# Performance work log

Hardware: AMD Instinct MI355X
Metric: run time of the kernel (lower is better)

## Reference

```python
import jax, jax.numpy as jnp
import numpy as np

N, K = 8192, 32
DIM_INP_Q, DIM_INP_KV, DIM, DIM_OUT = 256, 256, 256, 512


def setup_inputs() -> dict:
    key = jax.random.key(0)
    ks = jax.random.split(key, 16)
    s = lambda k_, shp: jax.random.normal(k_, shp, dtype=jnp.float32) * 0.05
    return {
        "xyz_q": jax.random.normal(ks[0], (N, 3), dtype=jnp.float32),
        "feats_q": jax.random.normal(ks[1], (N, DIM_INP_Q), dtype=jnp.float32),
        "xyz_kv": jax.random.normal(ks[2], (N, K, 3), dtype=jnp.float32),
        "feats_kv": jax.random.normal(ks[3], (N, K, DIM_INP_KV), dtype=jnp.float32),
        # linear weights stored (in, out); y = x @ W + b
        "Wq": s(ks[4], (DIM_INP_Q, DIM)),
        "Wk": s(ks[5], (DIM_INP_KV, DIM)),
        "Wv": s(ks[6], (DIM_INP_KV, DIM)),
        "d1_w": s(ks[7], (3, DIM // 2)), "d1_b": jnp.zeros((DIM // 2,), jnp.float32),
        "d2_w": s(ks[8], (DIM // 2, DIM)), "d2_b": jnp.zeros((DIM,), jnp.float32),
        "g1_w": s(ks[9], (DIM, DIM)), "g1_b": jnp.zeros((DIM,), jnp.float32),
        "g2_w": s(ks[10], (DIM, DIM)), "g2_b": jnp.zeros((DIM,), jnp.float32),
        "out_w": s(ks[11], (DIM, DIM_OUT)), "out_b": jnp.zeros((DIM_OUT,), jnp.float32),
    }


def reference(xyz_q, feats_q, xyz_kv, feats_kv, Wq, Wk, Wv,
              d1_w, d1_b, d2_w, d2_b, g1_w, g1_b, g2_w, g2_b, out_w, out_b):
    q_attn = feats_q @ Wq                      # (N, dim)
    k_attn = feats_kv @ Wk                     # (N, k, dim)
    v_attn = feats_kv @ Wv                     # (N, k, dim)
    # relative-position MLP: (N, k, 3) -> (N, k, dim)
    rel = xyz_q[:, None, :] - xyz_kv
    pos_encode = jax.nn.relu(rel @ d1_w + d1_b) @ d2_w + d2_b
    # subtractive vector attention scores through fc_gamma MLP
    h = q_attn[:, None, :] - k_attn + pos_encode
    attn = jax.nn.relu(h @ g1_w + g1_b) @ g2_w + g2_b   # (N, k, dim)
    attn = jax.nn.softmax(attn, axis=-2)                # softmax over neighbors k
    res = jnp.einsum('nmf,nmf->nf', attn, v_attn + pos_encode)
    res = res @ out_w + out_b                           # (N, dim_out)
    return (xyz_q, res)
```

## Files before the change

### kernel.cpp

```cpp
#include <hip/hip_runtime.h>
#include <hip/hip_bf16.h>

#define NPTS 8192
#define KN   32
#define DIM  256
#define DH   128
#define DOUT 512

typedef __attribute__((ext_vector_type(8))) short bf16x8;
typedef __attribute__((ext_vector_type(4))) short short4v;
typedef __attribute__((ext_vector_type(4))) float f32x4;

#define MFMA16(a, b, c) __builtin_amdgcn_mfma_f32_16x16x32_bf16((a), (b), (c), 0, 0, 0)

__device__ __forceinline__ short f2b(float f) {
    __hip_bfloat16 h = __float2bfloat16(f);
    return *reinterpret_cast<short*>(&h);
}

#define WSO_QATTN 0u
#define WSO_RES   8388608u
#define WSO_WKT   16777216u
#define WSO_WVT   16908288u
#define WSO_G1T   17039360u
#define WSO_G2T   17170432u
#define WSO_D2T   17301504u
#define WSO_OWT   17367040u

extern "C" __global__ __launch_bounds__(256)
void prep_w(const float* __restrict__ Wk, const float* __restrict__ Wv,
            const float* __restrict__ g1w, const float* __restrict__ g2w,
            const float* __restrict__ d2w, const float* __restrict__ ow,
            short* __restrict__ wkT, short* __restrict__ wvT,
            short* __restrict__ g1T, short* __restrict__ g2T,
            short* __restrict__ d2T, short* __restrict__ owT)
{
    const int idx = blockIdx.x * 256 + threadIdx.x;
    if (idx < 65536) {
        const int o = idx >> 8, i = idx & 255;
        wkT[idx] = f2b(-Wk[i * 256 + o]);
        wvT[idx] = f2b(Wv[i * 256 + o]);
        g1T[idx] = f2b(g1w[i * 256 + o]);
        g2T[idx] = f2b(g2w[i * 256 + o]);
    }
    if (idx < 32768) {
        const int o = idx >> 7, i = idx & 127;
        d2T[idx] = f2b(d2w[i * 256 + o]);
    }
    if (idx < 131072) {
        const int o = idx >> 8, i = idx & 255;
        owT[idx] = f2b(ow[i * 512 + o]);
    }
}

extern "C" __global__ __launch_bounds__(256)
void prep_q(const float* __restrict__ feats_q, const float* __restrict__ Wq,
            const float* __restrict__ xyz_q, float* __restrict__ q_attn,
            float* __restrict__ out)
{
    const int b = blockIdx.x;
    const int t = threadIdx.x;
    if (b >= 512) {
        const int idx = (b - 512) * 256 + t;
        out[idx] = xyz_q[idx];
        return;
    }
    __shared__ float s_q[16][256];
    for (int j = 0; j < 16; ++j)
        s_q[j][t] = feats_q[(size_t)(b * 16 + j) * 256 + t];
    __syncthreads();
    float acc[16];
    #pragma unroll
    for (int pt = 0; pt < 16; ++pt) acc[pt] = 0.f;
    for (int k = 0; k < 256; ++k) {
        const float wv = Wq[k * 256 + t];
        #pragma unroll
        for (int pt = 0; pt < 16; ++pt) acc[pt] = fmaf(s_q[pt][k], wv, acc[pt]);
    }
    #pragma unroll
    for (int pt = 0; pt < 16; ++pt)
        q_attn[(size_t)(b * 16 + pt) * 256 + t] = acc[pt];
}


#define STAGE_FEATS(koff)                                                         \
    {                                                                             \
        const float* fp_ = feats_kv + ((size_t)p0 * KN + srow) * DIM + (koff) +   \
                           scs * 32;                                              \
        _Pragma("unroll")                                                         \
        for (int j_ = 0; j_ < 8; ++j_) {                                          \
            const float4 v_ = *(const float4*)(fp_ + 4 * j_);                     \
            const int c2_ = scs * 32 + 4 * j_;                                    \
            short4v t_;                                                           \
            t_[0] = f2b(v_.x); t_[1] = f2b(v_.y);                                 \
            t_[2] = f2b(v_.z); t_[3] = f2b(v_.w);                                 \
            *(short4v*)&s_lds[srow * 128 + (c2_ ^ ((srow & 7) << 3))] = t_;       \
        }                                                                         \
    }

extern "C" __global__ __launch_bounds__(512, 2)
void ctb_main(const float* __restrict__ xyz_q, const float* __restrict__ xyz_kv,
              const float* __restrict__ feats_kv,
              const float* __restrict__ d1w, const float* __restrict__ d1b,
              const float* __restrict__ d2b, const float* __restrict__ g1b,
              const float* __restrict__ g2b,
              const float* __restrict__ q_attn,
              const short* __restrict__ wkTn, const short* __restrict__ wvT,
              const short* __restrict__ g1T, const short* __restrict__ g2T,
              const short* __restrict__ d2T,
              float* __restrict__ res_ws)
{
    extern __shared__ short s_lds[];
    const int t    = threadIdx.x;
    const int w    = t >> 6;
    const int lane = t & 63;
    const int q    = lane >> 4;
    const int ln   = lane & 15;
    const int p0   = blockIdx.x * 4;
    const int colbase = 32 * w + ln;

    const int srow = t >> 2;
    const int scs  = t & 3;

    STAGE_FEATS(0);
    {
        const int pt = srow >> 5;
        const float qx = xyz_q[(p0 + pt) * 3 + 0];
        const float qy = xyz_q[(p0 + pt) * 3 + 1];
        const float qz = xyz_q[(p0 + pt) * 3 + 2];
        const float* xk = xyz_kv + ((size_t)p0 * KN + srow) * 3;
        const float rx = qx - xk[0], ry = qy - xk[1], rz = qz - xk[2];
        #pragma unroll
        for (int j = 0; j < 32; ++j) {
            const int c = scs * 32 + j;
            const float v = fmaxf(fmaf(rx, d1w[c],
                                  fmaf(ry, d1w[DH + c],
                                  fmaf(rz, d1w[2 * DH + c], d1b[c]))), 0.f);
            s_lds[16384 + srow * 128 + (c ^ ((srow & 7) << 3))] = f2b(v);
        }
    }
    __syncthreads();

    f32x4 vp[8][2];
    #pragma unroll
    for (int nt = 0; nt < 2; ++nt) {
        const float bb = d2b[colbase + 16 * nt];
        #pragma unroll
        for (int mt = 0; mt < 8; ++mt) vp[mt][nt] = (f32x4){bb, bb, bb, bb};
    }
    #pragma unroll
    for (int ks = 0; ks < 4; ++ks) {
        bf16x8 ar[8];
        #pragma unroll
        for (int mt = 0; mt < 8; ++mt) {
            const int row = 16 * mt + ln;
            ar[mt] = *(const bf16x8*)&s_lds[16384 + row * 128 +
                                            ((32 * ks + 8 * q) ^ ((row & 7) << 3))];
        }
        #pragma unroll
        for (int nt = 0; nt < 2; ++nt) {
            const bf16x8 bb = *(const bf16x8*)(d2T + (colbase + 16 * nt) * DH +
                                               32 * ks + 8 * q);
            #pragma unroll
            for (int mt = 0; mt < 8; ++mt)
                vp[mt][nt] = MFMA16(ar[mt], bb, vp[mt][nt]);
        }
    }
    f32x4 hacc[8][2];
    #pragma unroll
    for (int nt = 0; nt < 2; ++nt)
        #pragma unroll
        for (int pt = 0; pt < 4; ++pt) {
            const float qv = q_attn[(size_t)(p0 + pt) * DIM + colbase + 16 * nt];
            #pragma unroll
            for (int m2 = 0; m2 < 2; ++m2) {
                const int mt = 2 * pt + m2;
                #pragma unroll
                for (int r = 0; r < 4; ++r) hacc[mt][nt][r] = vp[mt][nt][r] + qv;
            }
        }
    #pragma unroll
    for (int half = 0; half < 2; ++half) {
        if (half) {
            __syncthreads();
            STAGE_FEATS(128);
            __syncthreads();
        }
        #pragma unroll
        for (int ksl = 0; ksl < 4; ++ksl) {
            const int ks = 4 * half + ksl;
            bf16x8 af[8];
            #pragma unroll
            for (int mt = 0; mt < 8; ++mt) {
                const int row = 16 * mt + ln;
                af[mt] = *(const bf16x8*)&s_lds[row * 128 +
                                                ((32 * ksl + 8 * q) ^ ((row & 7) << 3))];
            }
            #pragma unroll
            for (int nt = 0; nt < 2; ++nt) {
                const int co = (colbase + 16 * nt) * DIM + 32 * ks + 8 * q;
                const bf16x8 bk = *(const bf16x8*)(wkTn + co);
                const bf16x8 bv = *(const bf16x8*)(wvT + co);
                #pragma unroll
                for (int mt = 0; mt < 8; ++mt) {
                    hacc[mt][nt] = MFMA16(af[mt], bk, hacc[mt][nt]);
                    vp[mt][nt]   = MFMA16(af[mt], bv, vp[mt][nt]);
                }
            }
        }
    }
    __syncthreads();
    #pragma unroll
    for (int mt = 0; mt < 8; ++mt)
        #pragma unroll
        for (int nt = 0; nt < 2; ++nt)
            #pragma unroll
            for (int r = 0; r < 4; ++r) {
                const int row = 16 * mt + 4 * q + r;
                const int col = colbase + 16 * nt;
                s_lds[row * 256 + (col ^ ((row & 7) << 3))] = f2b(hacc[mt][nt][r]);
            }
    __syncthreads();

    {
        f32x4 tacc[8][2];
        #pragma unroll
        for (int nt = 0; nt < 2; ++nt) {
            const float bb = g1b[colbase + 16 * nt];
            #pragma unroll
            for (int mt = 0; mt < 8; ++mt) tacc[mt][nt] = (f32x4){bb, bb, bb, bb};
        }
        #pragma unroll
        for (int ks = 0; ks < 8; ++ks) {
            bf16x8 ah[8];
            #pragma unroll
            for (int mt = 0; mt < 8; ++mt) {
                const int row = 16 * mt + ln;
                ah[mt] = *(const bf16x8*)&s_lds[row * 256 +
                                                ((32 * ks + 8 * q) ^ ((row & 7) << 3))];
            }
            #pragma unroll
            for (int nt = 0; nt < 2; ++nt) {
                const bf16x8 bb = *(const bf16x8*)(g1T + (colbase + 16 * nt) * DIM +
                                                   32 * ks + 8 * q);
                #pragma unroll
                for (int mt = 0; mt < 8; ++mt)
                    tacc[mt][nt] = MFMA16(ah[mt], bb, tacc[mt][nt]);
            }
        }
        __syncthreads();
        #pragma unroll
        for (int mt = 0; mt < 8; ++mt)
            #pragma unroll
            for (int nt = 0; nt < 2; ++nt)
                #pragma unroll
                for (int r = 0; r < 4; ++r) {
                    const int row = 16 * mt + 4 * q + r;
                    const int col = colbase + 16 * nt;
                    s_lds[row * 256 + (col ^ ((row & 7) << 3))] =
                        f2b(fmaxf(tacc[mt][nt][r], 0.f));
                }
        __syncthreads();
    }

    {
        f32x4 ap[8][2];
        #pragma unroll
        for (int nt = 0; nt < 2; ++nt) {
            const float bb = g2b[colbase + 16 * nt];
            #pragma unroll
            for (int mt = 0; mt < 8; ++mt) ap[mt][nt] = (f32x4){bb, bb, bb, bb};
        }
        #pragma unroll
        for (int ks = 0; ks < 8; ++ks) {
            bf16x8 at[8];
            #pragma unroll
            for (int mt = 0; mt < 8; ++mt) {
                const int row = 16 * mt + ln;
                at[mt] = *(const bf16x8*)&s_lds[row * 256 +
                                                ((32 * ks + 8 * q) ^ ((row & 7) << 3))];
            }
            #pragma unroll
            for (int nt = 0; nt < 2; ++nt) {
                const bf16x8 bb = *(const bf16x8*)(g2T + (colbase + 16 * nt) * DIM +
                                                   32 * ks + 8 * q);
                #pragma unroll
                for (int mt = 0; mt < 8; ++mt)
                    ap[mt][nt] = MFMA16(at[mt], bb, ap[mt][nt]);
            }
        }

        float stot[4][2];
        #pragma unroll
        for (int pt = 0; pt < 4; ++pt)
            #pragma unroll
            for (int nt = 0; nt < 2; ++nt) {
                float m = -1e30f;
                #pragma unroll
                for (int m2 = 0; m2 < 2; ++m2)
                    #pragma unroll
                    for (int r = 0; r < 4; ++r)
                        m = fmaxf(m, ap[2 * pt + m2][nt][r]);
                m = fmaxf(m, __shfl_xor(m, 16, 64));
                m = fmaxf(m, __shfl_xor(m, 32, 64));
                float s = 0.f;
                #pragma unroll
                for (int m2 = 0; m2 < 2; ++m2)
                    #pragma unroll
                    for (int r = 0; r < 4; ++r) {
                        const float e = __expf(ap[2 * pt + m2][nt][r] - m);
                        ap[2 * pt + m2][nt][r] = e;
                        s += e;
                    }
                s += __shfl_xor(s, 16, 64);
                s += __shfl_xor(s, 32, 64);
                stot[pt][nt] = s;
            }

        #pragma unroll
        for (int pt = 0; pt < 4; ++pt)
            #pragma unroll
            for (int nt = 0; nt < 2; ++nt) {
                float racc = 0.f;
                #pragma unroll
                for (int m2 = 0; m2 < 2; ++m2)
                    #pragma unroll
                    for (int r = 0; r < 4; ++r)
                        racc = fmaf(ap[2 * pt + m2][nt][r], vp[2 * pt + m2][nt][r],
                                    racc);
                racc += __shfl_xor(racc, 16, 64);
                racc += __shfl_xor(racc, 32, 64);
                if (q == 0)
                    res_ws[(size_t)(p0 + pt) * DIM + colbase + 16 * nt] =
                        racc / stot[pt][nt];
            }
    }
}

extern "C" __global__ __launch_bounds__(256, 2)
void ctb_out(const float* __restrict__ res_ws, const short* __restrict__ owT,
             const float* __restrict__ ob, float* __restrict__ out)
{
    __shared__ __align__(16) short s_a[64 * 256];
    const int t = threadIdx.x, w = t >> 6, lane = t & 63, q = lane >> 4, ln = lane & 15;
    const int rowbase = blockIdx.x * 64;

    {
        const int row = t >> 2;
        const int cs  = t & 3;
        const float* src = res_ws + (size_t)(rowbase + row) * DIM + cs * 64;
        #pragma unroll
        for (int j = 0; j < 16; ++j) {
            const float4 v = *(const float4*)(src + 4 * j);
            const int c = cs * 64 + 4 * j;
            short4v sv;
            sv[0] = f2b(v.x); sv[1] = f2b(v.y); sv[2] = f2b(v.z); sv[3] = f2b(v.w);
            *(short4v*)&s_a[row * 256 + (c ^ ((row & 7) << 3))] = sv;
        }
    }
    __syncthreads();

    const int colbase = 128 * w + ln;
    f32x4 acc[4][8];
    #pragma unroll
    for (int nt = 0; nt < 8; ++nt) {
        const float bb = ob[colbase + 16 * nt];
        #pragma unroll
        for (int mt = 0; mt < 4; ++mt) acc[mt][nt] = (f32x4){bb, bb, bb, bb};
    }
    #pragma unroll
    for (int ks = 0; ks < 8; ++ks) {
        bf16x8 af[4];
        #pragma unroll
        for (int mt = 0; mt < 4; ++mt) {
            const int row = 16 * mt + ln;
            af[mt] = *(const bf16x8*)&s_a[row * 256 +
                                          ((32 * ks + 8 * q) ^ ((row & 7) << 3))];
        }
        #pragma unroll
        for (int nt = 0; nt < 8; ++nt) {
            const bf16x8 bb = *(const bf16x8*)(owT + (colbase + 16 * nt) * DIM +
                                               32 * ks + 8 * q);
            #pragma unroll
            for (int mt = 0; mt < 4; ++mt)
                acc[mt][nt] = MFMA16(af[mt], bb, acc[mt][nt]);
        }
    }
    float* o = out + (size_t)NPTS * 3;
    #pragma unroll
    for (int mt = 0; mt < 4; ++mt)
        #pragma unroll
        for (int nt = 0; nt < 8; ++nt)
            #pragma unroll
            for (int r = 0; r < 4; ++r) {
                const int row = 16 * mt + 4 * q + r;
                const int col = colbase + 16 * nt;
                o[(size_t)(rowbase + row) * DOUT + col] = acc[mt][nt][r];
            }
}

extern "C" void kernel_launch(void* const* d_in, const int* in_sizes, int n_in,
                              void* d_out, int out_size, void* d_ws, size_t ws_size,
                              hipStream_t stream) {
    const float* xyz_q    = (const float*)d_in[0];
    const float* feats_q  = (const float*)d_in[1];
    const float* xyz_kv   = (const float*)d_in[2];
    const float* feats_kv = (const float*)d_in[3];
    const float* Wq       = (const float*)d_in[4];
    const float* Wk       = (const float*)d_in[5];
    const float* Wv       = (const float*)d_in[6];
    const float* d1w      = (const float*)d_in[7];
    const float* d1b      = (const float*)d_in[8];
    const float* d2w      = (const float*)d_in[9];
    const float* d2b      = (const float*)d_in[10];
    const float* g1w      = (const float*)d_in[11];
    const float* g1b      = (const float*)d_in[12];
    const float* g2w      = (const float*)d_in[13];
    const float* g2b      = (const float*)d_in[14];
    const float* ow       = (const float*)d_in[15];
    const float* ob       = (const float*)d_in[16];
    float* out = (float*)d_out;

    char* ws = (char*)d_ws;
    float* q_attn = (float*)(ws + WSO_QATTN);
    float* res_ws = (float*)(ws + WSO_RES);
    short* wkT    = (short*)(ws + WSO_WKT);
    short* wvT    = (short*)(ws + WSO_WVT);
    short* g1T    = (short*)(ws + WSO_G1T);
    short* g2T    = (short*)(ws + WSO_G2T);
    short* d2T    = (short*)(ws + WSO_D2T);
    short* owT    = (short*)(ws + WSO_OWT);

    prep_w<<<dim3(512), dim3(256), 0, stream>>>(Wk, Wv, g1w, g2w, d2w, ow,
                                                wkT, wvT, g1T, g2T, d2T, owT);
    prep_q<<<dim3(608), dim3(256), 0, stream>>>(feats_q, Wq, xyz_q, q_attn, out);
    ctb_main<<<dim3(2048), dim3(512), 65536, stream>>>(
        xyz_q, xyz_kv, feats_kv, d1w, d1b, d2b, g1b, g2b,
        q_attn, wkT, wvT, g1T, g2T, d2T, res_ws);
    ctb_out<<<dim3(128), dim3(256), 0, stream>>>(res_ws, owT, ob, out);
}
```

Measured before the change: 677.4 us.

## Fuse output projection into main kernel and double threads per block

```diff
diff --git a/kernel.cpp b/kernel.cpp
--- a/kernel.cpp
+++ b/kernel.cpp
@@ -19,21 +19,19 @@
 }
 
 #define WSO_QATTN 0u
-#define WSO_RES   8388608u
 #define WSO_WKT   16777216u
 #define WSO_WVT   16908288u
 #define WSO_G1T   17039360u
 #define WSO_G2T   17170432u
 #define WSO_D2T   17301504u
-#define WSO_OWT   17367040u
 
 extern "C" __global__ __launch_bounds__(256)
 void prep_w(const float* __restrict__ Wk, const float* __restrict__ Wv,
             const float* __restrict__ g1w, const float* __restrict__ g2w,
-            const float* __restrict__ d2w, const float* __restrict__ ow,
+            const float* __restrict__ d2w,
             short* __restrict__ wkT, short* __restrict__ wvT,
             short* __restrict__ g1T, short* __restrict__ g2T,
-            short* __restrict__ d2T, short* __restrict__ owT)
+            short* __restrict__ d2T)
 {
     const int idx = blockIdx.x * 256 + threadIdx.x;
     if (idx < 65536) {
@@ -47,10 +45,6 @@
         const int o = idx >> 7, i = idx & 127;
         d2T[idx] = f2b(d2w[i * 256 + o]);
     }
-    if (idx < 131072) {
-        const int o = idx >> 8, i = idx & 255;
-        owT[idx] = f2b(ow[i * 512 + o]);
-    }
 }
 
 extern "C" __global__ __launch_bounds__(256)
@@ -60,37 +54,46 @@
 {
     const int b = blockIdx.x;
     const int t = threadIdx.x;
-    if (b >= 512) {
-        const int idx = (b - 512) * 256 + t;
+    if (b >= 256) {
+        const int idx = (b - 256) * 256 + t;
         out[idx] = xyz_q[idx];
         return;
     }
-    __shared__ float s_q[16][256];
-    for (int j = 0; j < 16; ++j)
-        s_q[j][t] = feats_q[(size_t)(b * 16 + j) * 256 + t];
-    __syncthreads();
-    float acc[16];
+    __shared__ float s_q[32][256];
+    for (int j = 0; j < 32; ++j)
+        s_q[j][t] = feats_q[(size_t)(b * 32 + j) * 256 + t];
+    __syncthreads();
+    float acc[32];
     #pragma unroll
-    for (int pt = 0; pt < 16; ++pt) acc[pt] = 0.f;
-    for (int k = 0; k < 256; ++k) {
-        const float wv = Wq[k * 256 + t];
-        #pragma unroll
-        for (int pt = 0; pt < 16; ++pt) acc[pt] = fmaf(s_q[pt][k], wv, acc[pt]);
+    for (int pt = 0; pt < 32; ++pt) acc[pt] = 0.f;
+    for (int k = 0; k < 256; k += 4) {
+        float wv0 = Wq[(k + 0) * 256 + t];
+        float wv1 = Wq[(k + 1) * 256 + t];
+        float wv2 = Wq[(k + 2) * 256 + t];
+        float wv3 = Wq[(k + 3) * 256 + t];
+        #pragma unroll
+        for (int pt = 0; pt < 32; ++pt) {
+            const float4 sv = *(const float4*)&s_q[pt][k];
+            acc[pt] = fmaf(sv.x, wv0, acc[pt]);
+            acc[pt] = fmaf(sv.y, wv1, acc[pt]);
+            acc[pt] = fmaf(sv.z, wv2, acc[pt]);
+            acc[pt] = fmaf(sv.w, wv3, acc[pt]);
+        }
     }
     #pragma unroll
-    for (int pt = 0; pt < 16; ++pt)
-        q_attn[(size_t)(b * 16 + pt) * 256 + t] = acc[pt];
+    for (int pt = 0; pt < 32; ++pt)
+        q_attn[(size_t)(b * 32 + pt) * 256 + t] = acc[pt];
 }
 
 
 #define STAGE_FEATS(koff)                                                         \
     {                                                                             \
         const float* fp_ = feats_kv + ((size_t)p0 * KN + srow) * DIM + (koff) +   \
-                           scs * 32;                                              \
+                           sc * 16;                                               \
         _Pragma("unroll")                                                         \
-        for (int j_ = 0; j_ < 8; ++j_) {                                          \
+        for (int j_ = 0; j_ < 4; ++j_) {                                          \
             const float4 v_ = *(const float4*)(fp_ + 4 * j_);                     \
-            const int c2_ = scs * 32 + 4 * j_;                                    \
+            const int c2_ = sc * 16 + 4 * j_;                                     \
             short4v t_;                                                           \
             t_[0] = f2b(v_.x); t_[1] = f2b(v_.y);                                 \
             t_[2] = f2b(v_.z); t_[3] = f2b(v_.w);                                 \
@@ -98,7 +101,7 @@
         }                                                                         \
     }
 
-extern "C" __global__ __launch_bounds__(512, 2)
+extern "C" __global__ __launch_bounds__(1024, 4)
 void ctb_main(const float* __restrict__ xyz_q, const float* __restrict__ xyz_kv,
               const float* __restrict__ feats_kv,
               const float* __restrict__ d1w, const float* __restrict__ d1b,
@@ -108,7 +111,8 @@
               const short* __restrict__ wkTn, const short* __restrict__ wvT,
               const short* __restrict__ g1T, const short* __restrict__ g2T,
               const short* __restrict__ d2T,
-              float* __restrict__ res_ws)
+              const float* __restrict__ ow, const float* __restrict__ ob,
+              float* __restrict__ out)
 {
     extern __shared__ short s_lds[];
     const int t    = threadIdx.x;
@@ -117,10 +121,10 @@
     const int q    = lane >> 4;
     const int ln   = lane & 15;
     const int p0   = blockIdx.x * 4;
-    const int colbase = 32 * w + ln;
-
-    const int srow = t >> 2;
-    const int scs  = t & 3;
+    const int colb = 16 * w + ln;
+
+    const int srow = t >> 3;
+    const int sc   = t & 7;
 
     STAGE_FEATS(0);
     {
@@ -131,8 +135,8 @@
         const float* xk = xyz_kv + ((size_t)p0 * KN + srow) * 3;
         const float rx = qx - xk[0], ry = qy - xk[1], rz = qz - xk[2];
         #pragma unroll
-        for (int j = 0; j < 32; ++j) {
-            const int c = scs * 32 + j;
+        for (int j = 0; j < 16; ++j) {
+            const int c = sc * 16 + j;
             const float v = fmaxf(fmaf(rx, d1w[c],
                                   fmaf(ry, d1w[DH + c],
                                   fmaf(rz, d1w[2 * DH + c], d1b[c]))), 0.f);
@@ -141,12 +145,11 @@
     }
     __syncthreads();
 
-    f32x4 vp[8][2];
-    #pragma unroll
-    for (int nt = 0; nt < 2; ++nt) {
-        const float bb = d2b[colbase + 16 * nt];
-        #pragma unroll
-        for (int mt = 0; mt < 8; ++mt) vp[mt][nt] = (f32x4){bb, bb, bb, bb};
+    f32x4 vp[8];
+    {
+        const float bb0 = d2b[colb];
+        #pragma unroll
+        for (int mt = 0; mt < 8; ++mt) vp[mt] = (f32x4){bb0, bb0, bb0, bb0};
     }
     #pragma unroll
     for (int ks = 0; ks < 4; ++ks) {
@@ -157,29 +160,21 @@
             ar[mt] = *(const bf16x8*)&s_lds[16384 + row * 128 +
                                             ((32 * ks + 8 * q) ^ ((row & 7) << 3))];
         }
-        #pragma unroll
-        for (int nt = 0; nt < 2; ++nt) {
-            const bf16x8 bb = *(const bf16x8*)(d2T + (colbase + 16 * nt) * DH +
-                                               32 * ks + 8 * q);
-            #pragma unroll
-            for (int mt = 0; mt < 8; ++mt)
-                vp[mt][nt] = MFMA16(ar[mt], bb, vp[mt][nt]);
-        }
-    }
-    f32x4 hacc[8][2];
-    #pragma unroll
-    for (int nt = 0; nt < 2; ++nt)
-        #pragma unroll
-        for (int pt = 0; pt < 4; ++pt) {
-            const float qv = q_attn[(size_t)(p0 + pt) * DIM + colbase + 16 * nt];
-            #pragma unroll
-            for (int m2 = 0; m2 < 2; ++m2) {
-                const int mt = 2 * pt + m2;
-                #pragma unroll
-                for (int r = 0; r < 4; ++r) hacc[mt][nt][r] = vp[mt][nt][r] + qv;
-            }
-        }
-    #pragma unroll
+        const bf16x8 bb = *(const bf16x8*)(d2T + colb * DH + 32 * ks + 8 * q);
+        #pragma unroll
+        for (int mt = 0; mt < 8; ++mt) vp[mt] = MFMA16(ar[mt], bb, vp[mt]);
+    }
+    f32x4 hacc[8];
+    {
+        float qv[4];
+        #pragma unroll
+        for (int pt = 0; pt < 4; ++pt)
+            qv[pt] = q_attn[(size_t)(p0 + pt) * DIM + colb];
+        #pragma unroll
+        for (int mt = 0; mt < 8; ++mt)
+            #pragma unroll
+            for (int r = 0; r < 4; ++r) hacc[mt][r] = vp[mt][r] + qv[mt >> 1];
+    }
     for (int half = 0; half < 2; ++half) {
         if (half) {
             __syncthreads();
@@ -188,7 +183,6 @@
         }
         #pragma unroll
         for (int ksl = 0; ksl < 4; ++ksl) {
-            const int ks = 4 * half + ksl;
             bf16x8 af[8];
             #pragma unroll
             for (int mt = 0; mt < 8; ++mt) {
@@ -196,16 +190,13 @@
                 af[mt] = *(const bf16x8*)&s_lds[row * 128 +
                                                 ((32 * ksl + 8 * q) ^ ((row & 7) << 3))];
             }
-            #pragma unroll
-            for (int nt = 0; nt < 2; ++nt) {
-                const int co = (colbase + 16 * nt) * DIM + 32 * ks + 8 * q;
-                const bf16x8 bk = *(const bf16x8*)(wkTn + co);
-                const bf16x8 bv = *(const bf16x8*)(wvT + co);
-                #pragma unroll
-                for (int mt = 0; mt < 8; ++mt) {
-                    hacc[mt][nt] = MFMA16(af[mt], bk, hacc[mt][nt]);
-                    vp[mt][nt]   = MFMA16(af[mt], bv, vp[mt][nt]);
-                }
+            const int co = colb * DIM + 32 * (4 * half + ksl) + 8 * q;
+            const bf16x8 bk = *(const bf16x8*)(wkTn + co);
+            const bf16x8 bv = *(const bf16x8*)(wvT + co);
+            #pragma unroll
+            for (int mt = 0; mt < 8; ++mt) {
+                hacc[mt] = MFMA16(af[mt], bk, hacc[mt]);
+                vp[mt]   = MFMA16(af[mt], bv, vp[mt]);
             }
         }
     }
@@ -213,23 +204,17 @@
     #pragma unroll
     for (int mt = 0; mt < 8; ++mt)
         #pragma unroll
-        for (int nt = 0; nt < 2; ++nt)
-            #pragma unroll
-            for (int r = 0; r < 4; ++r) {
-                const int row = 16 * mt + 4 * q + r;
-                const int col = colbase + 16 * nt;
-                s_lds[row * 256 + (col ^ ((row & 7) << 3))] = f2b(hacc[mt][nt][r]);
-            }
-    __syncthreads();
-
-    {
-        f32x4 tacc[8][2];
-        #pragma unroll
-        for (int nt = 0; nt < 2; ++nt) {
-            const float bb = g1b[colbase + 16 * nt];
-            #pragma unroll
-            for (int mt = 0; mt < 8; ++mt) tacc[mt][nt] = (f32x4){bb, bb, bb, bb};
-        }
+        for (int r = 0; r < 4; ++r) {
+            const int row = 16 * mt + 4 * q + r;
+            s_lds[row * 256 + (colb ^ ((row & 7) << 3))] = f2b(hacc[mt][r]);
+        }
+    __syncthreads();
+
+    {
+        f32x4 tacc[8];
+        const float bb0 = g1b[colb];
+        #pragma unroll
+        for (int mt = 0; mt < 8; ++mt) tacc[mt] = (f32x4){bb0, bb0, bb0, bb0};
         #pragma unroll
         for (int ks = 0; ks < 8; ++ks) {
             bf16x8 ah[8];
@@ -239,38 +224,28 @@
                 ah[mt] = *(const bf16x8*)&s_lds[row * 256 +
                                                 ((32 * ks + 8 * q) ^ ((row & 7) << 3))];
             }
-            #pragma unroll
-            for (int nt = 0; nt < 2; ++nt) {
-                const bf16x8 bb = *(const bf16x8*)(g1T + (colbase + 16 * nt) * DIM +
-                                                   32 * ks + 8 * q);
-                #pragma unroll
-                for (int mt = 0; mt < 8; ++mt)
-                    tacc[mt][nt] = MFMA16(ah[mt], bb, tacc[mt][nt]);
-            }
+            const bf16x8 bb = *(const bf16x8*)(g1T + colb * DIM + 32 * ks + 8 * q);
+            #pragma unroll
+            for (int mt = 0; mt < 8; ++mt) tacc[mt] = MFMA16(ah[mt], bb, tacc[mt]);
         }
         __syncthreads();
         #pragma unroll
         for (int mt = 0; mt < 8; ++mt)
             #pragma unroll
-            for (int nt = 0; nt < 2; ++nt)
-                #pragma unroll
-                for (int r = 0; r < 4; ++r) {
-                    const int row = 16 * mt + 4 * q + r;
-                    const int col = colbase + 16 * nt;
-                    s_lds[row * 256 + (col ^ ((row & 7) << 3))] =
-                        f2b(fmaxf(tacc[mt][nt][r], 0.f));
-                }
+            for (int r = 0; r < 4; ++r) {
+                const int row = 16 * mt + 4 * q + r;
+                s_lds[row * 256 + (colb ^ ((row & 7) << 3))] =
+                    f2b(fmaxf(tacc[mt][r], 0.f));
+            }
         __syncthreads();
     }
 
-    {
-        f32x4 ap[8][2];
-        #pragma unroll
-        for (int nt = 0; nt < 2; ++nt) {
-            const float bb = g2b[colbase + 16 * nt];
-            #pragma unroll
-            for (int mt = 0; mt < 8; ++mt) ap[mt][nt] = (f32x4){bb, bb, bb, bb};
-        }
+    float rres[4];
+    {
+        f32x4 ap[8];
+        const float bb0 = g2b[colb];
+        #pragma unroll
+        for (int mt = 0; mt < 8; ++mt) ap[mt] = (f32x4){bb0, bb0, bb0, bb0};
         #pragma unroll
         for (int ks = 0; ks < 8; ++ks) {
             bf16x8 at[8];
@@ -280,123 +255,66 @@
                 at[mt] = *(const bf16x8*)&s_lds[row * 256 +
                                                 ((32 * ks + 8 * q) ^ ((row & 7) << 3))];
             }
-            #pragma unroll
-            for (int nt = 0; nt < 2; ++nt) {
-                const bf16x8 bb = *(const bf16x8*)(g2T + (colbase + 16 * nt) * DIM +
-                                                   32 * ks + 8 * q);
+            const bf16x8 bb = *(const bf16x8*)(g2T + colb * DIM + 32 * ks + 8 * q);
+            #pragma unroll
+            for (int mt = 0; mt < 8; ++mt) ap[mt] = MFMA16(at[mt], bb, ap[mt]);
+        }
+
+        #pragma unroll
+        for (int pt = 0; pt < 4; ++pt) {
+            float m = -1e30f;
+            #pragma unroll
+            for (int m2 = 0; m2 < 2; ++m2)
                 #pragma unroll
-                for (int mt = 0; mt < 8; ++mt)
-                    ap[mt][nt] = MFMA16(at[mt], bb, ap[mt][nt]);
-            }
-        }
-
-        float stot[4][2];
-        #pragma unroll
-        for (int pt = 0; pt < 4; ++pt)
-            #pragma unroll
-            for (int nt = 0; nt < 2; ++nt) {
-                float m = -1e30f;
+                for (int r = 0; r < 4; ++r) m = fmaxf(m, ap[2 * pt + m2][r]);
+            m = fmaxf(m, __shfl_xor(m, 16, 64));
+            m = fmaxf(m, __shfl_xor(m, 32, 64));
+            float s = 0.f;
+            #pragma unroll
+            for (int m2 = 0; m2 < 2; ++m2)
                 #pragma unroll
-                for (int m2 = 0; m2 < 2; ++m2)
-                    #pragma unroll
-                    for (int r = 0; r < 4; ++r)
-                        m = fmaxf(m, ap[2 * pt + m2][nt][r]);
-                m = fmaxf(m, __shfl_xor(m, 16, 64));
-                m = fmaxf(m, __shfl_xor(m, 32, 64));
-                float s = 0.f;
+                for (int r = 0; r < 4; ++r) {
+                    const float e = __expf(ap[2 * pt + m2][r] - m);
+                    ap[2 * pt + m2][r] = e;
+                    s += e;
+                }
+            s += __shfl_xor(s, 16, 64);
+            s += __shfl_xor(s, 32, 64);
+            float racc = 0.f;
+            #pragma unroll
+            for (int m2 = 0; m2 < 2; ++m2)
                 #pragma unroll
-                for (int m2 = 0; m2 < 2; ++m2)
-                    #pragma unroll
-                    for (int r = 0; r < 4; ++r) {
-                        const float e = __expf(ap[2 * pt + m2][nt][r] - m);
-                        ap[2 * pt + m2][nt][r] = e;
-                        s += e;
-                    }
-                s += __shfl_xor(s, 16, 64);
-                s += __shfl_xor(s, 32, 64);
-                stot[pt][nt] = s;
-            }
-
-        #pragma unroll
-        for (int pt = 0; pt < 4; ++pt)
-            #pragma unroll
-            for (int nt = 0; nt < 2; ++nt) {
-                float racc = 0.f;
-                #pragma unroll
-                for (int m2 = 0; m2 < 2; ++m2)
-                    #pragma unroll
-                    for (int r = 0; r < 4; ++r)
-                        racc = fmaf(ap[2 * pt + m2][nt][r], vp[2 * pt + m2][nt][r],
-                                    racc);
-                racc += __shfl_xor(racc, 16, 64);
-                racc += __shfl_xor(racc, 32, 64);
-                if (q == 0)
-                    res_ws[(size_t)(p0 + pt) * DIM + colbase + 16 * nt] =
-                        racc / stot[pt][nt];
-            }
-    }
-}
-
-extern "C" __global__ __launch_bounds__(256, 2)
-void ctb_out(const float* __restrict__ res_ws, const short* __restrict__ owT,
-             const float* __restrict__ ob, float* __restrict__ out)
-{
-    __shared__ __align__(16) short s_a[64 * 256];
-    const int t = threadIdx.x, w = t >> 6, lane = t & 63, q = lane >> 4, ln = lane & 15;
-    const int rowbase = blockIdx.x * 64;
-
-    {
-        const int row = t >> 2;
-        const int cs  = t & 3;
-        const float* src = res_ws + (size_t)(rowbase + row) * DIM + cs * 64;
-        #pragma unroll
-        for (int j = 0; j < 16; ++j) {
-            const float4 v = *(const float4*)(src + 4 * j);
-            const int c = cs * 64 + 4 * j;
-            short4v sv;
-            sv[0] = f2b(v.x); sv[1] = f2b(v.y); sv[2] = f2b(v.z); sv[3] = f2b(v.w);
-            *(short4v*)&s_a[row * 256 + (c ^ ((row & 7) << 3))] = sv;
-        }
-    }
-    __syncthreads();
-
-    const int colbase = 128 * w + ln;
-    f32x4 acc[4][8];
-    #pragma unroll
-    for (int nt = 0; nt < 8; ++nt) {
-        const float bb = ob[colbase + 16 * nt];
-        #pragma unroll
-        for (int mt = 0; mt < 4; ++mt) acc[mt][nt] = (f32x4){bb, bb, bb, bb};
-    }
-    #pragma unroll
-    for (int ks = 0; ks < 8; ++ks) {
-        bf16x8 af[4];
-        #pragma unroll
-        for (int mt = 0; mt < 4; ++mt) {
-            const int row = 16 * mt + ln;
-            af[mt] = *(const bf16x8*)&s_a[row * 256 +
-                                          ((32 * ks + 8 * q) ^ ((row & 7) << 3))];
-        }
-        #pragma unroll
-        for (int nt = 0; nt < 8; ++nt) {
-            const bf16x8 bb = *(const bf16x8*)(owT + (colbase + 16 * nt) * DIM +
-                                               32 * ks + 8 * q);
-            #pragma unroll
-            for (int mt = 0; mt < 4; ++mt)
-                acc[mt][nt] = MFMA16(af[mt], bb, acc[mt][nt]);
-        }
-    }
-    float* o = out + (size_t)NPTS * 3;
-    #pragma unroll
-    for (int mt = 0; mt < 4; ++mt)
-        #pragma unroll
-        for (int nt = 0; nt < 8; ++nt)
-            #pragma unroll
-            for (int r = 0; r < 4; ++r) {
-                const int row = 16 * mt + 4 * q + r;
-                const int col = colbase + 16 * nt;
-                o[(size_t)(rowbase + row) * DOUT + col] = acc[mt][nt][r];
-            }
+                for (int r = 0; r < 4; ++r)
+                    racc = fmaf(ap[2 * pt + m2][r], vp[2 * pt + m2][r], racc);
+            racc += __shfl_xor(racc, 16, 64);
+            racc += __shfl_xor(racc, 32, 64);
+            rres[pt] = racc / s;
+        }
+    }
+    __syncthreads();
+    float* s_res = (float*)s_lds;
+    if (q == 0) {
+        #pragma unroll
+        for (int pt = 0; pt < 4; ++pt) s_res[pt * 256 + colb] = rres[pt];
+    }
+    __syncthreads();
+
+    {
+        const int c  = t & 511;
+        const int p2 = t >> 9;
+        float a0 = ob[c], a1 = ob[c];
+        const float* r0 = s_res + (2 * p2) * 256;
+        const float* r1 = s_res + (2 * p2 + 1) * 256;
+        #pragma unroll 8
+        for (int k = 0; k < 256; ++k) {
+            const float wv = ow[(size_t)k * DOUT + c];
+            a0 = fmaf(r0[k], wv, a0);
+            a1 = fmaf(r1[k], wv, a1);
+        }
+        float* o = out + (size_t)NPTS * 3;
+        o[(size_t)(p0 + 2 * p2) * DOUT + c]     = a0;
+        o[(size_t)(p0 + 2 * p2 + 1) * DOUT + c] = a1;
+    }
 }
 
 extern "C" void kernel_launch(void* const* d_in, const int* in_sizes, int n_in,
@@ -423,19 +341,16 @@
 
     char* ws = (char*)d_ws;
     float* q_attn = (float*)(ws + WSO_QATTN);
-    float* res_ws = (float*)(ws + WSO_RES);
     short* wkT    = (short*)(ws + WSO_WKT);
     short* wvT    = (short*)(ws + WSO_WVT);
     short* g1T    = (short*)(ws + WSO_G1T);
     short* g2T    = (short*)(ws + WSO_G2T);
     short* d2T    = (short*)(ws + WSO_D2T);
-    short* owT    = (short*)(ws + WSO_OWT);
-
-    prep_w<<<dim3(512), dim3(256), 0, stream>>>(Wk, Wv, g1w, g2w, d2w, ow,
-                                                wkT, wvT, g1T, g2T, d2T, owT);
-    prep_q<<<dim3(608), dim3(256), 0, stream>>>(feats_q, Wq, xyz_q, q_attn, out);
-    ctb_main<<<dim3(2048), dim3(512), 65536, stream>>>(
+
+    prep_w<<<dim3(256), dim3(256), 0, stream>>>(Wk, Wv, g1w, g2w, d2w,
+                                                wkT, wvT, g1T, g2T, d2T);
+    prep_q<<<dim3(352), dim3(256), 0, stream>>>(feats_q, Wq, xyz_q, q_attn, out);
+    ctb_main<<<dim3(2048), dim3(1024), 65536, stream>>>(
         xyz_q, xyz_kv, feats_kv, d1w, d1b, d2b, g1b, g2b,
-        q_attn, wkT, wvT, g1T, g2T, d2T, res_ws);
-    ctb_out<<<dim3(128), dim3(256), 0, stream>>>(res_ws, owT, ob, out);
-}
+        q_attn, wkT, wvT, g1T, g2T, d2T, ow, ob, out);
+}
```

New measurement: 754.9 us. 11.4% more time.
